# Kernel optimization log

Measured on AMD Instinct MI355X. Metric: run time of the kernel, lower is better.

## Reference

```python
import jax, jax.numpy as jnp
import numpy as np

# Config constants from init_kwargs
DIM_GROUPS = [32, 32]   # hyper_cuts_dim_groups (sum == lsh_key_dim == d_key)
K_MAX = 64              # max candidates kept per query token


def _group_exact_match(qb, kb):
    """qb, kb: [B, L, d] binary {0,1} floats.
    Returns eq[b, i, j] = True iff all d bits of query i equal key j.
    Faithful to merge(Wu-Manber prefix match, Trie full-stride match):
    the Trie stores the full binary vector chunked by stride, so a Trie hit
    requires exact equality of the whole group's bit vector, which subsumes
    the Wu-Manber prefix condition; their intersection is exact equality.
    """
    # number of mismatching bits between query i and key j
    mism = (jnp.einsum('bid,bjd->bij', qb, 1.0 - kb)
            + jnp.einsum('bid,bjd->bij', 1.0 - qb, kb))
    return mism == 0.0


def setup_inputs() -> dict:
    key = jax.random.key(0)
    k1, k2 = jax.random.split(key)
    B, L, D = 4, 2048, 64
    return {
        'query_up': jax.random.normal(k1, (B, L, D), dtype=jnp.float32),
        'key_up': jax.random.normal(k2, (B, L, D), dtype=jnp.float32),
        'head_idx': 0,
    }


def reference(query_up, key_up, head_idx):
    B, L, _ = query_up.shape
    # binary_quantize: (x > 0).float()
    qb = (query_up > 0).astype(jnp.float32)
    kb = (key_up > 0).astype(jnp.float32)
    # per dim-group exact match (Wu-Manber \cap Trie), union across groups
    match = jnp.zeros((B, L, L), dtype=bool)
    start = 0
    for gd in DIM_GROUPS:
        match = match | _group_exact_match(qb[..., start:start + gd],
                                           kb[..., start:start + gd])
        start += gd
    # gather up to K_MAX smallest matching key indices per query, pad with -1
    idx = jnp.where(match, jnp.arange(L, dtype=jnp.int32)[None, None, :], L)
    cand = jnp.sort(idx, axis=-1)[..., :K_MAX]          # [B, L, K_MAX]
    return jnp.where(cand == L, -1, cand)
```

## Files before the change

### kernel.cpp

```cpp
#include <hip/hip_runtime.h>
#include <stdint.h>


#define LSEQ 2048
#define DDIM 64
#define KMAX 64

__global__ __launch_bounds__(256) void keysig_kernel(
    const float* __restrict__ key, uint2* __restrict__ ksig, int nrows) {
    int row  = (int)((blockIdx.x * blockDim.x + threadIdx.x) >> 6);
    int lane = threadIdx.x & 63;
    if (row >= nrows) return;
    float v = key[(size_t)row * DDIM + lane];
    unsigned long long m = __ballot(v > 0.0f);
    if (lane == 0) ksig[row] = make_uint2((unsigned)m, (unsigned)(m >> 32));
}

__global__ __launch_bounds__(256) void match_kernel(
    const float* __restrict__ query, const uint2* __restrict__ ksig,
    int* __restrict__ out, int nq) {
    int qid  = (int)((blockIdx.x * blockDim.x + threadIdx.x) >> 6);
    int lane = threadIdx.x & 63;
    if (qid >= nq) return;
    int b = qid >> 11;

    float v = query[(size_t)qid * DDIM + lane];
    unsigned long long qm = __ballot(v > 0.0f);
    unsigned q1 = (unsigned)qm, q2 = (unsigned)(qm >> 32);

    const uint2* ks = ksig + (size_t)b * LSEQ;
    int* obase = out + (size_t)qid * KMAX;
    unsigned long long below = (1ull << lane) - 1ull;

    int cnt = 0;
    for (int c = 0; c < LSEQ / 64; ++c) {
        uint2 kv = ks[c * 64 + lane];
        bool m = (kv.x == q1) || (kv.y == q2);
        unsigned long long mask = __ballot(m);
        if (mask) {
            if (m) {
                int pos = cnt + __popcll(mask & below);
                if (pos < KMAX) obase[pos] = c * 64 + lane;
            }
            cnt += __popcll(mask);
            if (cnt >= KMAX) break;
        }
    }
    if (lane >= cnt) obase[lane] = -1;
}

__global__ __launch_bounds__(256) void fused_kernel(
    const float* __restrict__ query, const float* __restrict__ key,
    int* __restrict__ out) {
    __shared__ uint2 ksig[LSEQ];
    const int blocksPerBatch = LSEQ / 64;
    int b    = blockIdx.x / blocksPerBatch;
    int qblk = blockIdx.x % blocksPerBatch;
    int lane = threadIdx.x & 63;
    int wave = threadIdx.x >> 6;

    const float* kb = key + (size_t)b * LSEQ * DDIM;
    for (int row = wave; row < LSEQ; row += 4) {
        float v = kb[(size_t)row * DDIM + lane];
        unsigned long long m = __ballot(v > 0.0f);
        if (lane == 0) ksig[row] = make_uint2((unsigned)m, (unsigned)(m >> 32));
    }
    __syncthreads();

    const float* qb = query + (size_t)b * LSEQ * DDIM;
    unsigned long long below = (1ull << lane) - 1ull;
    for (int t = 0; t < 16; ++t) {
        int qi = qblk * 64 + wave * 16 + t;
        float v = qb[(size_t)qi * DDIM + lane];
        unsigned long long qm = __ballot(v > 0.0f);
        unsigned q1 = (unsigned)qm, q2 = (unsigned)(qm >> 32);
        int* obase = out + ((size_t)b * LSEQ + qi) * KMAX;
        int cnt = 0;
        for (int c = 0; c < LSEQ / 64; ++c) {
            uint2 kv = ksig[c * 64 + lane];
            bool m = (kv.x == q1) || (kv.y == q2);
            unsigned long long mask = __ballot(m);
            if (mask) {
                if (m) {
                    int pos = cnt + __popcll(mask & below);
                    if (pos < KMAX) obase[pos] = c * 64 + lane;
                }
                cnt += __popcll(mask);
                if (cnt >= KMAX) break;
            }
        }
        if (lane >= cnt) obase[lane] = -1;
    }
}

extern "C" void kernel_launch(void* const* d_in, const int* in_sizes, int n_in,
                              void* d_out, int out_size, void* d_ws, size_t ws_size,
                              hipStream_t stream) {
    const float* q = (const float*)d_in[0];
    const float* k = (const float*)d_in[1];
    int* out = (int*)d_out;

    int total = in_sizes[0];
    int B = total / (LSEQ * DDIM);
    int nrows = B * LSEQ;

    size_t need = (size_t)nrows * sizeof(uint2);
    if (ws_size >= need) {
        uint2* ksig = (uint2*)d_ws;
        int threads = nrows * 64;
        keysig_kernel<<<(threads + 255) / 256, 256, 0, stream>>>(k, ksig, nrows);
        match_kernel<<<(threads + 255) / 256, 256, 0, stream>>>(q, ksig, out, nrows);
    } else {
        fused_kernel<<<B * (LSEQ / 64), 256, 0, stream>>>(q, k, out);
    }
}
```

Before: 70.16 us.

## Fuse key signature and matching into one kernel with float4 packed signatures

Replaces the two-kernel path (key signature to workspace, then matching) with a single kernel. Each block recomputes all key signatures of its batch into shared memory using float4 loads and shuffle-based bit packing, and handles 32 queries. The match loop is unrolled and drops the early break and the zero-mask branch. The cost is that every block recomputes the full key signature set, which adds redundant global reads.

```diff
diff --git a/kernel.cpp b/kernel.cpp
--- a/kernel.cpp
+++ b/kernel.cpp
@@ -5,89 +5,68 @@
 #define LSEQ 2048
 #define DDIM 64
 #define KMAX 64
+#define QPB  32
 
-__global__ __launch_bounds__(256) void keysig_kernel(
-    const float* __restrict__ key, uint2* __restrict__ ksig, int nrows) {
-    int row  = (int)((blockIdx.x * blockDim.x + threadIdx.x) >> 6);
-    int lane = threadIdx.x & 63;
-    if (row >= nrows) return;
-    float v = key[(size_t)row * DDIM + lane];
-    unsigned long long m = __ballot(v > 0.0f);
-    if (lane == 0) ksig[row] = make_uint2((unsigned)m, (unsigned)(m >> 32));
+__device__ __forceinline__ uint2 pack4rows(float4 v, int sub) {
+    unsigned n = (v.x > 0.f ? 1u : 0u) | (v.y > 0.f ? 2u : 0u)
+               | (v.z > 0.f ? 4u : 0u) | (v.w > 0.f ? 8u : 0u);
+    unsigned x = n << (4 * (sub & 7));
+    x |= __shfl_xor(x, 1);
+    x |= __shfl_xor(x, 2);
+    x |= __shfl_xor(x, 4);
+    unsigned y = __shfl_down(x, 8);
+    return make_uint2(x, y);
 }
 
-__global__ __launch_bounds__(256) void match_kernel(
-    const float* __restrict__ query, const uint2* __restrict__ ksig,
-    int* __restrict__ out, int nq) {
-    int qid  = (int)((blockIdx.x * blockDim.x + threadIdx.x) >> 6);
+__global__ __launch_bounds__(256) void cand_kernel(
+    const float* __restrict__ query, const float* __restrict__ key,
+    int* __restrict__ out) {
+    __shared__ uint2 ks[LSEQ];
+    __shared__ uint2 qs[QPB];
+
+    const int bpb  = LSEQ / QPB;
+    int b    = blockIdx.x / bpb;
+    int qblk = blockIdx.x % bpb;
     int lane = threadIdx.x & 63;
-    if (qid >= nq) return;
-    int b = qid >> 11;
+    int wave = threadIdx.x >> 6;
+    int sub  = lane & 15;
+    int rsub = lane >> 4;
 
-    float v = query[(size_t)qid * DDIM + lane];
-    unsigned long long qm = __ballot(v > 0.0f);
-    unsigned q1 = (unsigned)qm, q2 = (unsigned)(qm >> 32);
+    const float4* kb4 = (const float4*)(key + (size_t)b * LSEQ * DDIM);
+    for (int i = 0; i < LSEQ / 4 / 4; ++i) {
+        int row = wave * (LSEQ / 4) + i * 4 + rsub;
+        float4 v = kb4[row * 16 + sub];
+        uint2 s = pack4rows(v, sub);
+        if (sub == 0) ks[row] = s;
+    }
+    const float4* qb4 =
+        (const float4*)(query + ((size_t)b * LSEQ + (size_t)qblk * QPB) * DDIM);
+    for (int i = 0; i < QPB / 4 / 4 / 2; ++i) {
+    }
+    for (int i = 0; i < 2; ++i) {
+        int row = wave * 8 + i * 4 + rsub;
+        float4 v = qb4[row * 16 + sub];
+        uint2 s = pack4rows(v, sub);
+        if (sub == 0) qs[row] = s;
+    }
+    __syncthreads();
 
-    const uint2* ks = ksig + (size_t)b * LSEQ;
-    int* obase = out + (size_t)qid * KMAX;
     unsigned long long below = (1ull << lane) - 1ull;
-
-    int cnt = 0;
-    for (int c = 0; c < LSEQ / 64; ++c) {
-        uint2 kv = ks[c * 64 + lane];
-        bool m = (kv.x == q1) || (kv.y == q2);
-        unsigned long long mask = __ballot(m);
-        if (mask) {
+    for (int t = 0; t < QPB / 4; ++t) {
+        int ql = wave * (QPB / 4) + t;
+        uint2 q = qs[ql];
+        int* obase = out + ((size_t)b * LSEQ + (size_t)qblk * QPB + ql) * KMAX;
+        int cnt = 0;
+#pragma unroll 8
+        for (int c = 0; c < LSEQ / 64; ++c) {
+            uint2 kv = ks[c * 64 + lane];
+            bool m = (kv.x == q.x) || (kv.y == q.y);
+            unsigned long long mask = __ballot(m);
             if (m) {
                 int pos = cnt + __popcll(mask & below);
                 if (pos < KMAX) obase[pos] = c * 64 + lane;
             }
             cnt += __popcll(mask);
-            if (cnt >= KMAX) break;
-        }
-    }
-    if (lane >= cnt) obase[lane] = -1;
-}
-
-__global__ __launch_bounds__(256) void fused_kernel(
-    const float* __restrict__ query, const float* __restrict__ key,
-    int* __restrict__ out) {
-    __shared__ uint2 ksig[LSEQ];
-    const int blocksPerBatch = LSEQ / 64;
-    int b    = blockIdx.x / blocksPerBatch;
-    int qblk = blockIdx.x % blocksPerBatch;
-    int lane = threadIdx.x & 63;
-    int wave = threadIdx.x >> 6;
-
-    const float* kb = key + (size_t)b * LSEQ * DDIM;
-    for (int row = wave; row < LSEQ; row += 4) {
-        float v = kb[(size_t)row * DDIM + lane];
-        unsigned long long m = __ballot(v > 0.0f);
-        if (lane == 0) ksig[row] = make_uint2((unsigned)m, (unsigned)(m >> 32));
-    }
-    __syncthreads();
-
-    const float* qb = query + (size_t)b * LSEQ * DDIM;
-    unsigned long long below = (1ull << lane) - 1ull;
-    for (int t = 0; t < 16; ++t) {
-        int qi = qblk * 64 + wave * 16 + t;
-        float v = qb[(size_t)qi * DDIM + lane];
-        unsigned long long qm = __ballot(v > 0.0f);
-        unsigned q1 = (unsigned)qm, q2 = (unsigned)(qm >> 32);
-        int* obase = out + ((size_t)b * LSEQ + qi) * KMAX;
-        int cnt = 0;
-        for (int c = 0; c < LSEQ / 64; ++c) {
-            uint2 kv = ksig[c * 64 + lane];
-            bool m = (kv.x == q1) || (kv.y == q2);
-            unsigned long long mask = __ballot(m);
-            if (mask) {
-                if (m) {
-                    int pos = cnt + __popcll(mask & below);
-                    if (pos < KMAX) obase[pos] = c * 64 + lane;
-                }
-                cnt += __popcll(mask);
-                if (cnt >= KMAX) break;
-            }
         }
         if (lane >= cnt) obase[lane] = -1;
     }
@@ -102,15 +81,6 @@
 
     int total = in_sizes[0];
     int B = total / (LSEQ * DDIM);
-    int nrows = B * LSEQ;
 
-    size_t need = (size_t)nrows * sizeof(uint2);
-    if (ws_size >= need) {
-        uint2* ksig = (uint2*)d_ws;
-        int threads = nrows * 64;
-        keysig_kernel<<<(threads + 255) / 256, 256, 0, stream>>>(k, ksig, nrows);
-        match_kernel<<<(threads + 255) / 256, 256, 0, stream>>>(q, ksig, out, nrows);
-    } else {
-        fused_kernel<<<B * (LSEQ / 64), 256, 0, stream>>>(q, k, out);
-    }
+    cand_kernel<<<B * (LSEQ / QPB), 256, 0, stream>>>(q, k, out);
 }
```

Result: slower. 127.6 us (+81.9%).
